# Kernel optimization log

Measured on AMD Instinct MI355X. Metric: run time of the kernel, lower is better.

## Reference

```python
import jax, jax.numpy as jnp
import numpy as np

# Model dims (rexgen/WLN canonical hyperparameters)
B, N, MAXNB, NBONDS = 16, 100, 10, 120
AF, BF, H, BIN = 82, 6, 300, 11
DEPTH, K = 3, 80


def setup_inputs() -> dict:
    key = jax.random.key(0)
    ks = jax.random.split(key, 24)
    f32 = jnp.float32
    inp = {}
    inp["fatoms"] = jax.random.normal(ks[0], (B, N, AF), f32)
    inp["fbonds"] = jax.random.normal(ks[1], (B, NBONDS, BF), f32)
    inp["atom_nb"] = jax.random.randint(ks[2], (B, N, MAXNB), 0, N)
    inp["bond_nb"] = jax.random.randint(ks[3], (B, N, MAXNB), 0, NBONDS)
    inp["num_nbs"] = jnp.full((B, N), MAXNB, jnp.int32)
    inp["n_atoms"] = jnp.full((B,), N, jnp.int32)
    inp["binary_feats"] = jax.random.normal(ks[4], (B, N, N, BIN), f32)
    inp["mask_neis"] = (jax.random.uniform(ks[5], (B, N, MAXNB, 1)) > 0.2).astype(f32)
    inp["mask_atoms"] = jnp.ones((B, N, 1), f32)
    # sparse_idx enumerates all (sample, atom_i, atom_j) pairs in row-major order
    sb = jnp.repeat(jnp.arange(B), N * N)
    si = jnp.tile(jnp.repeat(jnp.arange(N), N), B)
    sj = jnp.tile(jnp.arange(N), B * N)
    inp["sparse_idx"] = jnp.stack([sb, si, sj], axis=1).astype(jnp.int32)

    def w(k, shape):
        return jax.random.normal(k, shape, f32) * 0.1

    # WLNet params
    inp["W_atom"] = w(ks[6], (AF, H))
    inp["W_nei_atom"] = w(ks[7], (H, H))
    inp["W_nei_bond"] = w(ks[8], (BF, H))
    inp["W_self"] = w(ks[9], (H, H))
    inp["W_U2"] = w(ks[10], (H + BF, H)); inp["b_U2"] = jnp.zeros((H,), f32)
    inp["W_U1"] = w(ks[11], (2 * H, H)); inp["b_U1"] = jnp.zeros((H,), f32)
    # Attention params
    inp["W_att_local"] = w(ks[12], (H, H))
    inp["W_att_bin"] = w(ks[13], (BIN, H)); inp["b_att"] = jnp.zeros((H,), f32)
    inp["W_att_score"] = w(ks[14], (H, 1)); inp["b_att_score"] = jnp.zeros((1,), f32)
    # ReactivityScoring params
    inp["W_pl"] = w(ks[15], (H, H))
    inp["W_pg"] = w(ks[16], (H, H))
    inp["W_pb"] = w(ks[17], (BIN, H)); inp["b_p"] = jnp.zeros((H,), f32)
    inp["W_out"] = w(ks[18], (H, 1)); inp["b_out"] = jnp.zeros((1,), f32)
    return inp


def _pair_scores(fatoms, fbonds, binary_feats, mask_neis, mask_atoms,
                 W_atom, W_nei_atom, W_nei_bond, W_self, W_U2, b_U2, W_U1, b_U1,
                 W_att_local, W_att_bin, b_att, W_att_score, b_att_score,
                 W_pl, W_pg, W_pb, b_p, W_out, b_out,
                 atom_nb, bond_nb, sparse_idx):
    bidx = jnp.arange(B)[:, None, None]
    # --- WLNet graph convolution ---
    h = jax.nn.relu(fatoms @ W_atom)                       # [B,N,H]
    local = h
    for _ in range(DEPTH):
        fnei_atom = h[bidx, atom_nb]                       # [B,N,MAXNB,H]
        fnei_bond = fbonds[bidx, bond_nb]                  # [B,N,MAXNB,BF]
        h_nei = (fnei_atom @ W_nei_atom) * (fnei_bond @ W_nei_bond)
        f_nei = (h_nei * mask_neis).sum(axis=2)            # [B,N,H]
        f_self = h @ W_self
        local = f_nei * f_self * mask_atoms                # kernel output
        nei_label = jax.nn.relu(jnp.concatenate([fnei_atom, fnei_bond], -1) @ W_U2 + b_U2)
        nei_label = (nei_label * mask_neis).sum(axis=2)
        h = jax.nn.relu(jnp.concatenate([h, nei_label], -1) @ W_U1 + b_U1)
    # --- Global attention over atom pairs ---
    pair = local[:, :, None, :] + local[:, None, :, :]     # [B,N,N,H]
    att_h = jax.nn.relu(pair @ W_att_local + binary_feats @ W_att_bin + b_att)
    att_s = jax.nn.sigmoid(att_h @ W_att_score + b_att_score)  # [B,N,N,1]
    ctx = jnp.einsum('bij,bjh->bih', att_s[..., 0], local)     # [B,N,H]
    # --- Gather sparse pairs and score reactivity ---
    sb, si, sj = sparse_idx[:, 0], sparse_idx[:, 1], sparse_idx[:, 2]
    local_pair = local[sb, si] + local[sb, sj]             # [P,H]
    global_pair = ctx[sb, si] + ctx[sb, sj]                # [P,H]
    bin_pair = binary_feats[sb, si, sj]                    # [P,BIN]
    hid = jax.nn.relu(local_pair @ W_pl + global_pair @ W_pg + bin_pair @ W_pb + b_p)
    return hid @ W_out + b_out                             # [P,1]


def reference(fatoms, fbonds, atom_nb, bond_nb, num_nbs, n_atoms, binary_feats,
              mask_neis, mask_atoms, sparse_idx,
              W_atom, W_nei_atom, W_nei_bond, W_self, W_U2, b_U2, W_U1, b_U1,
              W_att_local, W_att_bin, b_att, W_att_score, b_att_score,
              W_pl, W_pg, W_pb, b_p, W_out, b_out):
    pair_scores = _pair_scores(fatoms, fbonds, binary_feats, mask_neis, mask_atoms,
                               W_atom, W_nei_atom, W_nei_bond, W_self, W_U2, b_U2, W_U1, b_U1,
                               W_att_local, W_att_bin, b_att, W_att_score, b_att_score,
                               W_pl, W_pg, W_pb, b_p, W_out, b_out,
                               atom_nb, bond_nb, sparse_idx)
    # Segmented top-k: sparse_idx rows are grouped & ordered by sample with
    # exactly N*N pairs each, so per-sample flatten == reshape to [B, N*N].
    _, topks = jax.lax.top_k(pair_scores.reshape(B, N * N), K)  # indices, matching torch.topk[1]
    return pair_scores, topks
```

## Files before the change

kernel.cpp:

```cpp
#include <hip/hip_runtime.h>
#include <hip/hip_bf16.h>
#include <math.h>

#define BB 16
#define NN 100
#define MAXNB 10
#define NBONDS 120
#define AF 82
#define BF 6
#define HH 300
#define BIN 11
#define DEPTH 3
#define KTOP 80

typedef __attribute__((ext_vector_type(8))) short short8;
typedef __attribute__((ext_vector_type(4))) float floatx4;

__device__ __forceinline__ unsigned short f2bf(float f) {
    unsigned int u = __float_as_uint(f);
    unsigned int r = (u + 0x7FFFu + ((u >> 16) & 1u)) >> 16;
    return (unsigned short)r;
}
__device__ __forceinline__ float bf2f(unsigned short h) {
    return __uint_as_float(((unsigned int)h) << 16);
}

#define O_WATOM 0
#define O_WNB   29184
#define O_U2B   38912
#define O_WNA   48640
#define O_U2A   145920
#define O_WSELF 243200
#define O_U1A   340480
#define O_U1B   437760
#define O_WATT  535040
#define O_WPL   632320
#define O_WPG   729600

__global__ __launch_bounds__(256) void k_prep(
    const float* __restrict__ s0, const float* __restrict__ s1,
    const float* __restrict__ s2, const float* __restrict__ s3,
    const float* __restrict__ s4, const float* __restrict__ s5,
    const float* __restrict__ s6, const float* __restrict__ s7,
    const float* __restrict__ s8, const float* __restrict__ s9,
    const float* __restrict__ s10,
    unsigned short* __restrict__ WTh, unsigned short* __restrict__ WTl,
    const float* __restrict__ fatoms, const float* __restrict__ fbonds,
    unsigned short* __restrict__ fatomsbf, unsigned short* __restrict__ fbondsbf,
    const float* __restrict__ bin, unsigned short* __restrict__ BINBF,
    const float* __restrict__ Wbin0, const float* __restrict__ Wbin1,
    unsigned short* __restrict__ WBF0, unsigned short* __restrict__ WBF1)
{
    const int z = blockIdx.z;
    if (z == 11) {
        int idx = blockIdx.x * 256 + threadIdx.x;
        if (idx < 1600 * 96) {
            int r = idx / 96, c = idx - r * 96;
            float f = (c < AF) ? fatoms[r * AF + c] : 0.f;
            unsigned short hb = f2bf(f);
            fatomsbf[r * 192 + c]      = hb;
            fatomsbf[r * 192 + 96 + c] = f2bf(f - bf2f(hb));
        } else {
            int i2 = idx - 1600 * 96;
            if (i2 < 1920 * 32) {
                int r = i2 / 32, c = i2 - r * 32;
                float f = (c < BF) ? fbonds[r * BF + c] : 0.f;
                unsigned short hb = f2bf(f);
                fbondsbf[r * 64 + c]      = hb;
                fbondsbf[r * 64 + 32 + c] = f2bf(f - bf2f(hb));
            }
        }
        return;
    }
    if (z == 12) {
        const int bx = blockIdx.x;
        if (bx < 625) {
            int p = bx * 256 + threadIdx.x;
            if (p < BB * NN * NN) {
                const float* src = bin + (size_t)p * BIN;
                unsigned short tmp[16];
#pragma unroll
                for (int k = 0; k < BIN; k++) tmp[k] = f2bf(src[k]);
#pragma unroll
                for (int k = BIN; k < 16; k++) tmp[k] = 0;
                *(uint4*)(BINBF + (size_t)p * 16) = *(uint4*)tmp;
                *(uint4*)(BINBF + (size_t)p * 16 + 8) = *(uint4*)(tmp + 8);
            }
        } else if (bx < 663) {
            int zb = bx - 625;
            const float* src = (zb >= 19) ? Wbin1 : Wbin0;
            unsigned short* dst = (zb >= 19) ? WBF1 : WBF0;
            int idx = (zb % 19) * 256 + threadIdx.x;
            int jj = idx & 7;
            int koct = (idx >> 3) & 1;
            int n = (idx >> 4) & 15;
            int ch = idx >> 8;
            int k = koct * 8 + jj;
            int h = ch * 16 + n;
            float f = (k < BIN && h < 300) ? src[k * 300 + h] : 0.f;
            dst[idx] = f2bf(f);
        }
        return;
    }
    const float* src; int K, kc, off;
    switch (z) {
        case 0:  src = s0;  K = AF;  kc = 3;  off = O_WATOM; break;
        case 1:  src = s1;  K = BF;  kc = 1;  off = O_WNB;   break;
        case 2:  src = s2;  K = BF;  kc = 1;  off = O_U2B;   break;
        case 3:  src = s3;  K = HH;  kc = 10; off = O_WNA;   break;
        case 4:  src = s4;  K = HH;  kc = 10; off = O_U2A;   break;
        case 5:  src = s5;  K = HH;  kc = 10; off = O_WSELF; break;
        case 6:  src = s6;  K = HH;  kc = 10; off = O_U1A;   break;
        case 7:  src = s7;  K = HH;  kc = 10; off = O_U1B;   break;
        case 8:  src = s8;  K = HH;  kc = 10; off = O_WATT;  break;
        case 9:  src = s9;  K = HH;  kc = 10; off = O_WPL;   break;
        default: src = s10; K = HH;  kc = 10; off = O_WPG;   break;
    }
    const int lim = 9728 * kc;
    int i = blockIdx.x * 256 + threadIdx.x;
    if (i < lim) {
        int jj = i & 7;
        int lane = (i >> 3) & 63;
        int rem = i >> 9;
        int kci = rem % kc;
        int ct = rem / kc;
        int k = kci * 32 + (lane >> 4) * 8 + jj;
        int col = ct * 16 + (lane & 15);
        float f = (k < K && col < 300) ? src[k * 300 + col] : 0.f;
        unsigned short hb = f2bf(f);
        WTh[off + i] = hb;
        WTl[off + i] = f2bf(f - bf2f(hb));
    }
}

__device__ __forceinline__ void gemm_core(
    const unsigned short* __restrict__ A, int lda, int kc, int M,
    const unsigned short* __restrict__ wthB, const unsigned short* __restrict__ wtlB,
    float* __restrict__ C, int ldc,
    const float* __restrict__ bias,
    const float* __restrict__ Add, int ldAdd, int addOff,
    int act, unsigned short* __restrict__ Cbf,
    int row0, int gcolBase)
{
    __shared__ unsigned short sa[16 * 648];
    if (row0 >= M) return;
    const int tid = threadIdx.x;
    const int lane = tid & 63;
    const int wid = tid >> 6;
    const int sR = kc * 64 + 8;

    {
        const uint4* Ag = (const uint4*)A;
        uint4* sa4 = (uint4*)sa;
        const int q4 = kc * 8;
        const int lda4 = lda >> 3;
        const int sR4 = q4 + 1;
        for (int i = tid; i < 16 * q4; i += 256) {
            int r = i / q4, q = i - r * q4;
            sa4[r * sR4 + q] = Ag[(size_t)(row0 + r) * lda4 + q];
        }
    }
    __syncthreads();

    const int ct = blockIdx.y * 4 + wid;
    if (ct >= 19) return;

    const int m = lane & 15;
    const int rq = lane >> 4;
    const int koct8 = rq * 8;
    const unsigned short* wth = wthB + (size_t)ct * kc * 512;
    const unsigned short* wtl = wtlB + (size_t)ct * kc * 512;

    floatx4 acc = {0.f, 0.f, 0.f, 0.f};
    for (int kci = 0; kci < kc; kci++) {
        short8 ah = *(const short8*)(sa + m * sR + kci * 32 + koct8);
        short8 al = *(const short8*)(sa + m * sR + kc * 32 + kci * 32 + koct8);
        short8 wh = *(const short8*)(wth + (kci * 64 + lane) * 8);
        short8 wl = *(const short8*)(wtl + (kci * 64 + lane) * 8);
        acc = __builtin_amdgcn_mfma_f32_16x16x32_bf16(ah, wl, acc, 0, 0, 0);
        acc = __builtin_amdgcn_mfma_f32_16x16x32_bf16(al, wh, acc, 0, 0, 0);
        acc = __builtin_amdgcn_mfma_f32_16x16x32_bf16(ah, wh, acc, 0, 0, 0);
    }

    const int col = ct * 16 + m;
    if (col < 300) {
        const float bv = bias ? bias[col] : 0.f;
        const int gcol = gcolBase + col;
#pragma unroll
        for (int r = 0; r < 4; r++) {
            const int grow = row0 + rq * 4 + r;
            float v = acc[r] + bv;
            if (Add) v += Add[(size_t)grow * ldAdd + addOff + col];
            if (act) v = fmaxf(v, 0.f);
            if (C) C[(size_t)grow * ldc + gcol] = v;
            if (Cbf) {
                unsigned short hb = f2bf(v);
                Cbf[(size_t)grow * 640 + col]       = hb;
                Cbf[(size_t)grow * 640 + 320 + col] = f2bf(v - bf2f(hb));
            }
        }
    }
}

__global__ __launch_bounds__(256) void k_gemm_mfma(
    const unsigned short* __restrict__ A, int lda, int kc, int M,
    const unsigned short* __restrict__ WTh, const unsigned short* __restrict__ WTl,
    int wtStride,
    float* __restrict__ C, int ldc,
    const float* __restrict__ bias,
    const float* __restrict__ Add, int ldAdd, int addOff,
    int act, unsigned short* __restrict__ Cbf)
{
    const int widx = blockIdx.z;
    gemm_core(A, lda, kc, M,
              WTh + (size_t)widx * wtStride, WTl + (size_t)widx * wtStride,
              C, ldc, bias, Add, ldAdd, addOff, act, Cbf,
              blockIdx.x * 16, widx * 300);
}

__global__ __launch_bounds__(256) void k_gemm_first(
    const unsigned short* __restrict__ fatomsbf,
    const unsigned short* __restrict__ fbondsbf,
    const unsigned short* __restrict__ WTh, const unsigned short* __restrict__ WTl,
    unsigned short* __restrict__ hbf, float* __restrict__ FBout)
{
    const int z = blockIdx.z;
    if (z == 0) {
        gemm_core(fatomsbf, 192, 3, 1600,
                  WTh + O_WATOM, WTl + O_WATOM,
                  nullptr, 0, nullptr, nullptr, 0, 0, 1, hbf,
                  blockIdx.x * 16, 0);
    } else {
        const int w = z - 1;
        gemm_core(fbondsbf, 64, 1, 1920,
                  WTh + O_WNB + w * 9728, WTl + O_WNB + w * 9728,
                  FBout, 600, nullptr, nullptr, 0, 0, 0, nullptr,
                  blockIdx.x * 16, w * 300);
    }
}

__global__ __launch_bounds__(320) void k_neighbor(
    const float* __restrict__ HW, const float* __restrict__ FB,
    const int* __restrict__ atom_nb, const int* __restrict__ bond_nb,
    const float* __restrict__ mask_neis, const float* __restrict__ mask_atoms,
    const float* __restrict__ b_U2,
    unsigned short* __restrict__ localbf, unsigned short* __restrict__ nlbf)
{
    __shared__ int   sAn[4][MAXNB];
    __shared__ int   sBd[4][MAXNB];
    __shared__ float sM[4][MAXNB];
    const int tx = threadIdx.x;
    const int ty = threadIdx.y;
    const int bx = blockIdx.x;
    const int bn0 = ((bx & 15) * 25 + (bx >> 4)) * 4;
    const int flat = ty * 80 + tx;

    if (flat < 40)        sAn[flat / 10][flat % 10] = atom_nb[(bn0 + flat / 10) * MAXNB + flat % 10];
    else if (flat < 80)  { int f = flat - 40; sBd[f / 10][f % 10] = bond_nb[(bn0 + f / 10) * MAXNB + f % 10]; }
    else if (flat < 120) { int f = flat - 80; sM[f / 10][f % 10]  = mask_neis[(bn0 + f / 10) * MAXNB + f % 10]; }
    __syncthreads();

    if (tx >= 75) return;
    const int bn = bn0 + ty;
    const int b = bn / NN;
    const int h4 = tx;

    const float4* HW4 = (const float4*)HW;
    const float4* FB4 = (const float4*)FB;
    const float4 bu = ((const float4*)b_U2)[h4];

    float4 fnei = make_float4(0.f,0.f,0.f,0.f);
    float4 nls  = fnei;
#pragma unroll
    for (int k = 0; k < MAXNB; k++) {
        const int an = sAn[ty][k];
        const int bd = sBd[ty][k];
        const float m = sM[ty][k];
        const float4* hr = HW4 + (size_t)(b * NN + an) * 300;
        const float4* fr = FB4 + (size_t)(b * NBONDS + bd) * 150;
        float4 ha = hr[h4];
        float4 hu = hr[75 + h4];
        float4 fa = fr[h4];
        float4 fu = fr[75 + h4];
        fnei.x = fmaf(m, ha.x * fa.x, fnei.x);
        fnei.y = fmaf(m, ha.y * fa.y, fnei.y);
        fnei.z = fmaf(m, ha.z * fa.z, fnei.z);
        fnei.w = fmaf(m, ha.w * fa.w, fnei.w);
        float ux = hu.x + fu.x + bu.x;
        float uy = hu.y + fu.y + bu.y;
        float uz = hu.z + fu.z + bu.z;
        float uw = hu.w + fu.w + bu.w;
        nls.x = fmaf(m, fmaxf(ux, 0.f), nls.x);
        nls.y = fmaf(m, fmaxf(uy, 0.f), nls.y);
        nls.z = fmaf(m, fmaxf(uz, 0.f), nls.z);
        nls.w = fmaf(m, fmaxf(uw, 0.f), nls.w);
    }
    const float ma = mask_atoms[bn];
    const float4 sf = HW4[(size_t)bn * 300 + 150 + h4];
    float lv[4], nv[4];
    lv[0] = fnei.x * sf.x * ma; lv[1] = fnei.y * sf.y * ma;
    lv[2] = fnei.z * sf.z * ma; lv[3] = fnei.w * sf.w * ma;
    nv[0] = nls.x; nv[1] = nls.y; nv[2] = nls.z; nv[3] = nls.w;

    ushort4 lh, ll, nh, nl2;
    unsigned short* lhp = (unsigned short*)&lh;
    unsigned short* llp = (unsigned short*)&ll;
    unsigned short* nhp = (unsigned short*)&nh;
    unsigned short* nlp = (unsigned short*)&nl2;
#pragma unroll
    for (int c = 0; c < 4; c++) {
        unsigned short hb = f2bf(lv[c]);
        lhp[c] = hb; llp[c] = f2bf(lv[c] - bf2f(hb));
        unsigned short nb = f2bf(nv[c]);
        nhp[c] = nb; nlp[c] = f2bf(nv[c] - bf2f(nb));
    }
    *(ushort4*)(localbf + (size_t)bn * 640 + h4 * 4)       = lh;
    *(ushort4*)(localbf + (size_t)bn * 640 + 320 + h4 * 4) = ll;
    *(ushort4*)(nlbf    + (size_t)bn * 640 + h4 * 4)       = nh;
    *(ushort4*)(nlbf    + (size_t)bn * 640 + 320 + h4 * 4) = nl2;
}

__global__ __launch_bounds__(256) void k_pair(
    const float* __restrict__ R, int ldr,
    const unsigned short* __restrict__ BINBF,
    const unsigned short* __restrict__ WBF,
    const float* __restrict__ bvec,
    const float* __restrict__ Wscore, const float* __restrict__ bscore,
    float* __restrict__ outp, int mode)
{
    __shared__ float sLi[16 * 308];
    __shared__ float sLj[16 * 308];

    const int b  = blockIdx.x;
    const int i0 = blockIdx.y * 16;
    const int j0 = blockIdx.z * 16;
    const int tid = threadIdx.x;
    const int lane = tid & 63;
    const int wid = tid >> 6;

    for (int idx = tid; idx < 16 * 308; idx += 256) {
        int r = idx / 308;
        int c = idx - r * 308;
        float vi = 0.f, vj = 0.f;
        if (c < 300) {
            if (i0 + r < NN) vi = R[(size_t)(b * NN + i0 + r) * ldr + c] + bvec[c];
            if (j0 + r < NN) vj = R[(size_t)(b * NN + j0 + r) * ldr + c];
        }
        sLi[idx] = vi;
        sLj[idx] = vj;
    }

    const int m = lane & 15;
    const int koct = lane >> 4;
    short8 afrag[4];
#pragma unroll
    for (int g = 0; g < 4; g++) {
        int ii = i0 + wid * 4 + g; if (ii > NN - 1) ii = NN - 1;
        int jj2 = j0 + m;          if (jj2 > NN - 1) jj2 = NN - 1;
        const size_t pidx = (size_t)((b * NN + ii) * NN + jj2);
        afrag[g] = *(const short8*)(BINBF + pidx * 16 + (koct & 1) * 8);
        if (koct >= 2) afrag[g] = short8{0,0,0,0,0,0,0,0};
    }
    __syncthreads();

    const int n = lane & 15;
    const int rquad = lane >> 4;
    const floatx4 zero = {0.f, 0.f, 0.f, 0.f};
    float su[4][4];
#pragma unroll
    for (int g = 0; g < 4; g++)
#pragma unroll
        for (int r = 0; r < 4; r++) su[g][r] = 0.f;

    for (int ch = 0; ch < 19; ch++) {
        const int h0 = ch * 16;
        short8 bfrag = {0,0,0,0,0,0,0,0};
        if (lane < 32)
            bfrag = *(const short8*)(WBF + ch * 256 + (n * 2 + koct) * 8);
        float wsv = 0.f;
        if (h0 + n < 300) wsv = Wscore[h0 + n];
#pragma unroll
        for (int g = 0; g < 4; g++) {
            floatx4 P = __builtin_amdgcn_mfma_f32_16x16x32_bf16(
                afrag[g], bfrag, zero, 0, 0, 0);
            const float liv = sLi[(wid * 4 + g) * 308 + h0 + n];
#pragma unroll
            for (int r = 0; r < 4; r++) {
                const float ljv = sLj[(rquad * 4 + r) * 308 + h0 + n];
                float u = P[r] + liv + ljv;
                su[g][r] = fmaf(fmaxf(u, 0.f), wsv, su[g][r]);
            }
        }
    }

    const float bs = bscore[0];
#pragma unroll
    for (int g = 0; g < 4; g++) {
#pragma unroll
        for (int r = 0; r < 4; r++) {
            float v = su[g][r];
            v += __shfl_xor(v, 1);
            v += __shfl_xor(v, 2);
            v += __shfl_xor(v, 4);
            v += __shfl_xor(v, 8);
            if (n == 0) {
                const int i = i0 + wid * 4 + g;
                const int j = j0 + rquad * 4 + r;
                if (i < NN && j < NN) {
                    float s = v + bs;
                    outp[(size_t)(b * NN + i) * NN + j] =
                        (mode == 0) ? (1.f / (1.f + expf(-s))) : s;
                }
            }
        }
    }
}

__global__ __launch_bounds__(320) void k_ctx(
    const float* __restrict__ att, const unsigned short* __restrict__ localbf,
    unsigned short* __restrict__ ctxbf)
{
    const int bx = blockIdx.x;
    const int b = bx & 15;
    const int i0 = (bx >> 4) * 4;
    const int tid = threadIdx.x;
    __shared__ float sa[4 * NN];
    for (int idx = tid; idx < 4 * NN; idx += 320) {
        int ii = idx / NN, j = idx - ii * NN;
        sa[idx] = att[(size_t)(b * NN + i0 + ii) * NN + j];
    }
    __syncthreads();
    if (tid < HH) {
        float acc0 = 0.f, acc1 = 0.f, acc2 = 0.f, acc3 = 0.f;
        for (int j = 0; j < NN; j++) {
            const unsigned short* lr = localbf + (size_t)(b * NN + j) * 640;
            float lv = bf2f(lr[tid]) + bf2f(lr[320 + tid]);
            acc0 = fmaf(sa[j], lv, acc0);
            acc1 = fmaf(sa[NN + j], lv, acc1);
            acc2 = fmaf(sa[2 * NN + j], lv, acc2);
            acc3 = fmaf(sa[3 * NN + j], lv, acc3);
        }
        float vals[4] = {acc0, acc1, acc2, acc3};
#pragma unroll
        for (int k = 0; k < 4; k++) {
            unsigned short hb = f2bf(vals[k]);
            ctxbf[(size_t)(b * NN + i0 + k) * 640 + tid]       = hb;
            ctxbf[(size_t)(b * NN + i0 + k) * 640 + 320 + tid] = f2bf(vals[k] - bf2f(hb));
        }
    }
}

__global__ __launch_bounds__(1024) void k_topk(
    const float* __restrict__ scores, float* __restrict__ topk_out)
{
    const int b = blockIdx.x;
    const int tid = threadIdx.x;
    const int wid = tid >> 6;
    const int lane = tid & 63;
    const float* sc = scores + (size_t)b * (NN * NN);

    __shared__ unsigned int skey[NN * NN];
    __shared__ unsigned int whist[16 * 256];
    __shared__ unsigned int hist[256];
    __shared__ unsigned int candU[KTOP];
    __shared__ int candI[KTOP];
    __shared__ int cntG;
    __shared__ int curMin;
    __shared__ unsigned int sh_pref, sh_mask;
    __shared__ int sh_kRem;
    __shared__ int sh_last;

    for (int idx = tid; idx < NN * NN; idx += 1024) {
        unsigned int u = __float_as_uint(sc[idx]);
        u = (u & 0x80000000u) ? ~u : (u | 0x80000000u);
        skey[idx] = u;
    }
    if (tid == 0) {
        sh_pref = 0u; sh_mask = 0u; sh_kRem = KTOP; cntG = 0; sh_last = -1;
    }
    __syncthreads();

    for (int pass = 0; pass < 4; pass++) {
        const int shift = 24 - 8 * pass;
        unsigned int* wh = whist + (wid << 8);
        wh[lane] = 0u; wh[lane + 64] = 0u; wh[lane + 128] = 0u; wh[lane + 192] = 0u;
        __syncthreads();
        const unsigned int pref = sh_pref, mask = sh_mask;
        for (int idx = tid; idx < NN * NN; idx += 1024) {
            unsigned int u = skey[idx];
            if ((u & mask) == pref)
                atomicAdd(&wh[(u >> shift) & 255u], 1u);
        }
        __syncthreads();
        if (tid < 256) {
            unsigned int s = 0u;
#pragma unroll
            for (int w = 0; w < 16; w++) s += whist[(w << 8) | tid];
            hist[tid] = s;
        }
        __syncthreads();
        if (wid == 0) {
            unsigned int h0 = hist[lane * 4 + 0];
            unsigned int h1 = hist[lane * 4 + 1];
            unsigned int h2 = hist[lane * 4 + 2];
            unsigned int h3 = hist[lane * 4 + 3];
            unsigned int own = h0 + h1 + h2 + h3;
            unsigned int suf = own;
#pragma unroll
            for (int off = 1; off < 64; off <<= 1) {
                unsigned int v = __shfl_down(suf, off);
                if (lane + off < 64) suf += v;
            }
            const int k = sh_kRem;
            const unsigned int above = suf - own;
            if (above < (unsigned int)k && suf >= (unsigned int)k) {
                unsigned int c = above, hb; int bsel;
                c += h3;
                if ((int)c >= k) { bsel = lane * 4 + 3; hb = h3; }
                else { c += h2;
                    if ((int)c >= k) { bsel = lane * 4 + 2; hb = h2; }
                    else { c += h1;
                        if ((int)c >= k) { bsel = lane * 4 + 1; hb = h1; }
                        else { c += h0; bsel = lane * 4; hb = h0; } } }
                sh_kRem = k - (int)(c - hb);
                sh_pref = pref | ((unsigned int)bsel << shift);
                sh_mask = mask | (0xFFu << shift);
            }
        }
        __syncthreads();
    }
    const unsigned int T = sh_pref;

    for (int idx = tid; idx < NN * NN; idx += 1024) {
        unsigned int u = skey[idx];
        if (u > T) {
            int pos = atomicAdd(&cntG, 1);
            candU[pos] = u;
            candI[pos] = idx;
        }
    }
    __syncthreads();
    const int needE = KTOP - cntG;

    for (int e = 0; e < needE; e++) {
        if (tid == 0) curMin = 0x7fffffff;
        __syncthreads();
        const int last = sh_last;
        for (int idx = tid; idx < NN * NN; idx += 1024) {
            if (skey[idx] == T && idx > last)
                atomicMin(&curMin, idx);
        }
        __syncthreads();
        if (tid == 0) {
            candU[cntG + e] = T;
            candI[cntG + e] = curMin;
            sh_last = curMin;
        }
        __syncthreads();
    }

    if (tid < KTOP) {
        const unsigned int mu = candU[tid];
        const int mi = candI[tid];
        int rank = 0;
        for (int o = 0; o < KTOP; o++) {
            unsigned int ou = candU[o];
            int oi = candI[o];
            if (ou > mu || (ou == mu && oi < mi)) rank++;
        }
        topk_out[b * KTOP + rank] = (float)mi;
    }
}

extern "C" void kernel_launch(void* const* d_in, const int* in_sizes, int n_in,
                              void* d_out, int out_size, void* d_ws, size_t ws_size,
                              hipStream_t stream) {
    const float* fatoms       = (const float*)d_in[0];
    const float* fbonds       = (const float*)d_in[1];
    const int*   atom_nb      = (const int*)d_in[2];
    const int*   bond_nb      = (const int*)d_in[3];
    const float* binary_feats = (const float*)d_in[6];
    const float* mask_neis    = (const float*)d_in[7];
    const float* mask_atoms   = (const float*)d_in[8];
    const float* W_atom       = (const float*)d_in[10];
    const float* W_nei_atom   = (const float*)d_in[11];
    const float* W_nei_bond   = (const float*)d_in[12];
    const float* W_self       = (const float*)d_in[13];
    const float* W_U2         = (const float*)d_in[14];
    const float* b_U2         = (const float*)d_in[15];
    const float* W_U1         = (const float*)d_in[16];
    const float* b_U1         = (const float*)d_in[17];
    const float* W_att_local  = (const float*)d_in[18];
    const float* W_att_bin    = (const float*)d_in[19];
    const float* b_att        = (const float*)d_in[20];
    const float* W_att_score  = (const float*)d_in[21];
    const float* b_att_score  = (const float*)d_in[22];
    const float* W_pl         = (const float*)d_in[23];
    const float* W_pg         = (const float*)d_in[24];
    const float* W_pb         = (const float*)d_in[25];
    const float* b_p          = (const float*)d_in[26];
    const float* W_out        = (const float*)d_in[27];
    const float* b_out        = (const float*)d_in[28];

    float* ws = (float*)d_ws;
    float* HW  = ws;
    float* FB  = HW + 1920000;
    float* LL  = FB + 1152000;
    float* LPG = LL + 960000;
    float* att = LPG + 480000;
    unsigned short* S0       = (unsigned short*)(ws + 4672000);
    unsigned short* hbf      = S0;
    unsigned short* nlbf     = S0 + 1024000;
    unsigned short* localbf  = S0 + 2048000;
    unsigned short* WTh      = S0 + 3072000;
    unsigned short* WTl      = S0 + 3898880;
    unsigned short* ctxbf    = S0 + 4725760;
    unsigned short* BINBF    = S0 + 5749760;
    unsigned short* WBF_att  = S0 + 8309760;
    unsigned short* WBF_fin  = S0 + 8314624;
    unsigned short* fatomsbf = S0 + 8319488;
    unsigned short* fbondsbf = S0 + 8626688;

    float* out = (float*)d_out;
    float* topk_out = out + (size_t)BB * NN * NN;

    k_prep<<<dim3(840, 1, 13), 256, 0, stream>>>(
        W_atom, W_nei_bond, W_U2 + 300 * 300, W_nei_atom, W_U2, W_self,
        W_U1, W_U1 + 300 * 300, W_att_local, W_pl, W_pg, WTh, WTl,
        fatoms, fbonds, fatomsbf, fbondsbf,
        binary_feats, BINBF, W_att_bin, W_pb, WBF_att, WBF_fin);

    k_gemm_first<<<dim3(120, 5, 3), 256, 0, stream>>>(
        fatomsbf, fbondsbf, WTh, WTl, hbf, FB);

    for (int d = 0; d < DEPTH; d++) {
        int nW = (d == DEPTH - 1) ? 3 : 4;
        k_gemm_mfma<<<dim3(104, 5, nW), 256, 0, stream>>>(
            hbf, 640, 10, 1600, WTh + O_WNA, WTl + O_WNA, 97280,
            HW, 1200, nullptr, nullptr, 0, 0, 0, nullptr);
        k_neighbor<<<dim3(400), dim3(80, 4), 0, stream>>>(
            HW, FB, atom_nb, bond_nb, mask_neis, mask_atoms, b_U2,
            localbf, nlbf);
        if (d < DEPTH - 1) {
            k_gemm_mfma<<<dim3(104, 5, 1), 256, 0, stream>>>(
                nlbf, 640, 10, 1600, WTh + O_U1B, WTl + O_U1B, 0,
                nullptr, 0, b_U1, HW, 1200, 900, 1, hbf);
        }
    }

    k_gemm_mfma<<<dim3(104, 5, 2), 256, 0, stream>>>(
        localbf, 640, 10, 1600, WTh + O_WATT, WTl + O_WATT, 97280,
        LL, 600, nullptr, nullptr, 0, 0, 0, nullptr);

    k_pair<<<dim3(16, 7, 7), 256, 0, stream>>>(
        LL, 600, BINBF, WBF_att, b_att, W_att_score, b_att_score,
        att, 0);

    k_ctx<<<dim3(BB * 25), 320, 0, stream>>>(att, localbf, ctxbf);

    k_gemm_mfma<<<dim3(104, 5, 1), 256, 0, stream>>>(
        ctxbf, 640, 10, 1600, WTh + O_WPG, WTl + O_WPG, 0,
        LPG, 300, nullptr, LL, 600, 300, 0, nullptr);

    k_pair<<<dim3(16, 7, 7), 256, 0, stream>>>(
        LPG, 300, BINBF, WBF_fin, b_p, W_out, b_out,
        out, 1);

    k_topk<<<dim3(BB), 1024, 0, stream>>>(out, topk_out);
}
```

Baseline: 295.4 us.

## Fuse U1 matmul into neighbor kernel and reassociate context projection

The U1 neighbor-label GEMM is folded into the neighbor aggregation kernel: each block stages its 4 rows of summed neighbor labels in shared memory and multiplies them by the FP32 W_U1 lower half with scalar FMAs. This removes a separate bf16-split MFMA launch per depth and the nlbf round trip. The context projection is reassociated as att·(local·W_pg), so W_pg joins the batched local GEMM and k_ctx writes LPG directly, dropping the ctx GEMM launch and its buffer. The last depth also skips the unused U2 neighbor path. In exchange, each of the 400 neighbor blocks re-streams the full 300x300 weight matrix through scalar FMAs, and the summation order changes.

```diff
diff --git a/kernel.cpp b/kernel.cpp
--- a/kernel.cpp
+++ b/kernel.cpp
@@ -43,7 +43,6 @@
     const float* __restrict__ s4, const float* __restrict__ s5,
     const float* __restrict__ s6, const float* __restrict__ s7,
     const float* __restrict__ s8, const float* __restrict__ s9,
-    const float* __restrict__ s10,
     unsigned short* __restrict__ WTh, unsigned short* __restrict__ WTl,
     const float* __restrict__ fatoms, const float* __restrict__ fbonds,
     unsigned short* __restrict__ fatomsbf, unsigned short* __restrict__ fbondsbf,
@@ -52,7 +51,7 @@
     unsigned short* __restrict__ WBF0, unsigned short* __restrict__ WBF1)
 {
     const int z = blockIdx.z;
-    if (z == 11) {
+    if (z == 10) {
         int idx = blockIdx.x * 256 + threadIdx.x;
         if (idx < 1600 * 96) {
             int r = idx / 96, c = idx - r * 96;
@@ -72,7 +71,7 @@
         }
         return;
     }
-    if (z == 12) {
+    if (z == 11) {
         const int bx = blockIdx.x;
         if (bx < 625) {
             int p = bx * 256 + threadIdx.x;
@@ -111,10 +110,9 @@
         case 4:  src = s4;  K = HH;  kc = 10; off = O_U2A;   break;
         case 5:  src = s5;  K = HH;  kc = 10; off = O_WSELF; break;
         case 6:  src = s6;  K = HH;  kc = 10; off = O_U1A;   break;
-        case 7:  src = s7;  K = HH;  kc = 10; off = O_U1B;   break;
-        case 8:  src = s8;  K = HH;  kc = 10; off = O_WATT;  break;
-        case 9:  src = s9;  K = HH;  kc = 10; off = O_WPL;   break;
-        default: src = s10; K = HH;  kc = 10; off = O_WPG;   break;
+        case 7:  src = s7;  K = HH;  kc = 10; off = O_WATT;  break;
+        case 8:  src = s8;  K = HH;  kc = 10; off = O_WPL;   break;
+        default: src = s9;  K = HH;  kc = 10; off = O_WPG;   break;
     }
     const int lim = 9728 * kc;
     int i = blockIdx.x * 256 + threadIdx.x;
@@ -243,12 +241,15 @@
     const float* __restrict__ HW, const float* __restrict__ FB,
     const int* __restrict__ atom_nb, const int* __restrict__ bond_nb,
     const float* __restrict__ mask_neis, const float* __restrict__ mask_atoms,
-    const float* __restrict__ b_U2,
-    unsigned short* __restrict__ localbf, unsigned short* __restrict__ nlbf)
+    const float* __restrict__ b_U2, const float* __restrict__ WU1B,
+    const float* __restrict__ b_U1,
+    unsigned short* __restrict__ localbf, unsigned short* __restrict__ hbf,
+    int computeU1)
 {
     __shared__ int   sAn[4][MAXNB];
     __shared__ int   sBd[4][MAXNB];
     __shared__ float sM[4][MAXNB];
+    __shared__ float sNL[4][300];
     const int tx = threadIdx.x;
     const int ty = threadIdx.y;
     const int bx = blockIdx.x;
@@ -260,64 +261,91 @@
     else if (flat < 120) { int f = flat - 80; sM[f / 10][f % 10]  = mask_neis[(bn0 + f / 10) * MAXNB + f % 10]; }
     __syncthreads();
 
-    if (tx >= 75) return;
-    const int bn = bn0 + ty;
-    const int b = bn / NN;
-    const int h4 = tx;
-
-    const float4* HW4 = (const float4*)HW;
-    const float4* FB4 = (const float4*)FB;
-    const float4 bu = ((const float4*)b_U2)[h4];
-
-    float4 fnei = make_float4(0.f,0.f,0.f,0.f);
-    float4 nls  = fnei;
-#pragma unroll
-    for (int k = 0; k < MAXNB; k++) {
-        const int an = sAn[ty][k];
-        const int bd = sBd[ty][k];
-        const float m = sM[ty][k];
-        const float4* hr = HW4 + (size_t)(b * NN + an) * 300;
-        const float4* fr = FB4 + (size_t)(b * NBONDS + bd) * 150;
-        float4 ha = hr[h4];
-        float4 hu = hr[75 + h4];
-        float4 fa = fr[h4];
-        float4 fu = fr[75 + h4];
-        fnei.x = fmaf(m, ha.x * fa.x, fnei.x);
-        fnei.y = fmaf(m, ha.y * fa.y, fnei.y);
-        fnei.z = fmaf(m, ha.z * fa.z, fnei.z);
-        fnei.w = fmaf(m, ha.w * fa.w, fnei.w);
-        float ux = hu.x + fu.x + bu.x;
-        float uy = hu.y + fu.y + bu.y;
-        float uz = hu.z + fu.z + bu.z;
-        float uw = hu.w + fu.w + bu.w;
-        nls.x = fmaf(m, fmaxf(ux, 0.f), nls.x);
-        nls.y = fmaf(m, fmaxf(uy, 0.f), nls.y);
-        nls.z = fmaf(m, fmaxf(uz, 0.f), nls.z);
-        nls.w = fmaf(m, fmaxf(uw, 0.f), nls.w);
-    }
-    const float ma = mask_atoms[bn];
-    const float4 sf = HW4[(size_t)bn * 300 + 150 + h4];
-    float lv[4], nv[4];
-    lv[0] = fnei.x * sf.x * ma; lv[1] = fnei.y * sf.y * ma;
-    lv[2] = fnei.z * sf.z * ma; lv[3] = fnei.w * sf.w * ma;
-    nv[0] = nls.x; nv[1] = nls.y; nv[2] = nls.z; nv[3] = nls.w;
-
-    ushort4 lh, ll, nh, nl2;
-    unsigned short* lhp = (unsigned short*)&lh;
-    unsigned short* llp = (unsigned short*)&ll;
-    unsigned short* nhp = (unsigned short*)&nh;
-    unsigned short* nlp = (unsigned short*)&nl2;
-#pragma unroll
-    for (int c = 0; c < 4; c++) {
-        unsigned short hb = f2bf(lv[c]);
-        lhp[c] = hb; llp[c] = f2bf(lv[c] - bf2f(hb));
-        unsigned short nb = f2bf(nv[c]);
-        nhp[c] = nb; nlp[c] = f2bf(nv[c] - bf2f(nb));
-    }
-    *(ushort4*)(localbf + (size_t)bn * 640 + h4 * 4)       = lh;
-    *(ushort4*)(localbf + (size_t)bn * 640 + 320 + h4 * 4) = ll;
-    *(ushort4*)(nlbf    + (size_t)bn * 640 + h4 * 4)       = nh;
-    *(ushort4*)(nlbf    + (size_t)bn * 640 + 320 + h4 * 4) = nl2;
+    if (tx < 75) {
+        const int bn = bn0 + ty;
+        const int b = bn / NN;
+        const int h4 = tx;
+
+        const float4* HW4 = (const float4*)HW;
+        const float4* FB4 = (const float4*)FB;
+        const float4 bu = ((const float4*)b_U2)[h4];
+
+        float4 fnei = make_float4(0.f,0.f,0.f,0.f);
+        float4 nls  = fnei;
+#pragma unroll
+        for (int k = 0; k < MAXNB; k++) {
+            const int an = sAn[ty][k];
+            const int bd = sBd[ty][k];
+            const float m = sM[ty][k];
+            const float4* hr = HW4 + (size_t)(b * NN + an) * 300;
+            const float4* fr = FB4 + (size_t)(b * NBONDS + bd) * 150;
+            float4 ha = hr[h4];
+            float4 fa = fr[h4];
+            fnei.x = fmaf(m, ha.x * fa.x, fnei.x);
+            fnei.y = fmaf(m, ha.y * fa.y, fnei.y);
+            fnei.z = fmaf(m, ha.z * fa.z, fnei.z);
+            fnei.w = fmaf(m, ha.w * fa.w, fnei.w);
+            if (computeU1) {
+                float4 hu = hr[75 + h4];
+                float4 fu = fr[75 + h4];
+                float ux = hu.x + fu.x + bu.x;
+                float uy = hu.y + fu.y + bu.y;
+                float uz = hu.z + fu.z + bu.z;
+                float uw = hu.w + fu.w + bu.w;
+                nls.x = fmaf(m, fmaxf(ux, 0.f), nls.x);
+                nls.y = fmaf(m, fmaxf(uy, 0.f), nls.y);
+                nls.z = fmaf(m, fmaxf(uz, 0.f), nls.z);
+                nls.w = fmaf(m, fmaxf(uw, 0.f), nls.w);
+            }
+        }
+        const float ma = mask_atoms[bn];
+        const float4 sf = HW4[(size_t)bn * 300 + 150 + h4];
+        float lv[4];
+        lv[0] = fnei.x * sf.x * ma; lv[1] = fnei.y * sf.y * ma;
+        lv[2] = fnei.z * sf.z * ma; lv[3] = fnei.w * sf.w * ma;
+
+        ushort4 lh, ll;
+        unsigned short* lhp = (unsigned short*)&lh;
+        unsigned short* llp = (unsigned short*)&ll;
+#pragma unroll
+        for (int c = 0; c < 4; c++) {
+            unsigned short hb = f2bf(lv[c]);
+            lhp[c] = hb; llp[c] = f2bf(lv[c] - bf2f(hb));
+        }
+        *(ushort4*)(localbf + (size_t)bn * 640 + h4 * 4)       = lh;
+        *(ushort4*)(localbf + (size_t)bn * 640 + 320 + h4 * 4) = ll;
+
+        if (computeU1) {
+            sNL[ty][h4 * 4 + 0] = nls.x;
+            sNL[ty][h4 * 4 + 1] = nls.y;
+            sNL[ty][h4 * 4 + 2] = nls.z;
+            sNL[ty][h4 * 4 + 3] = nls.w;
+        }
+    }
+    if (!computeU1) return;
+    __syncthreads();
+
+    if (flat < 300) {
+        float a0 = 0.f, a1 = 0.f, a2 = 0.f, a3 = 0.f;
+#pragma unroll 4
+        for (int k = 0; k < 300; k++) {
+            const float w = WU1B[k * 300 + flat];
+            a0 = fmaf(sNL[0][k], w, a0);
+            a1 = fmaf(sNL[1][k], w, a1);
+            a2 = fmaf(sNL[2][k], w, a2);
+            a3 = fmaf(sNL[3][k], w, a3);
+        }
+        const float bb = b_U1[flat];
+        float av[4] = {a0, a1, a2, a3};
+#pragma unroll
+        for (int r = 0; r < 4; r++) {
+            float v = HW[(size_t)(bn0 + r) * 1200 + 900 + flat] + bb + av[r];
+            v = fmaxf(v, 0.f);
+            unsigned short hb = f2bf(v);
+            hbf[(size_t)(bn0 + r) * 640 + flat]       = hb;
+            hbf[(size_t)(bn0 + r) * 640 + 320 + flat] = f2bf(v - bf2f(hb));
+        }
+    }
 }
 
 __global__ __launch_bounds__(256) void k_pair(
@@ -417,8 +445,8 @@
 }
 
 __global__ __launch_bounds__(320) void k_ctx(
-    const float* __restrict__ att, const unsigned short* __restrict__ localbf,
-    unsigned short* __restrict__ ctxbf)
+    const float* __restrict__ att, const float* __restrict__ LL,
+    float* __restrict__ LPG)
 {
     const int bx = blockIdx.x;
     const int b = bx & 15;
@@ -433,8 +461,7 @@
     if (tid < HH) {
         float acc0 = 0.f, acc1 = 0.f, acc2 = 0.f, acc3 = 0.f;
         for (int j = 0; j < NN; j++) {
-            const unsigned short* lr = localbf + (size_t)(b * NN + j) * 640;
-            float lv = bf2f(lr[tid]) + bf2f(lr[320 + tid]);
+            const float lv = LL[(size_t)(b * NN + j) * 900 + 600 + tid];
             acc0 = fmaf(sa[j], lv, acc0);
             acc1 = fmaf(sa[NN + j], lv, acc1);
             acc2 = fmaf(sa[2 * NN + j], lv, acc2);
@@ -443,9 +470,8 @@
         float vals[4] = {acc0, acc1, acc2, acc3};
 #pragma unroll
         for (int k = 0; k < 4; k++) {
-            unsigned short hb = f2bf(vals[k]);
-            ctxbf[(size_t)(b * NN + i0 + k) * 640 + tid]       = hb;
-            ctxbf[(size_t)(b * NN + i0 + k) * 640 + 320 + tid] = f2bf(vals[k] - bf2f(hb));
+            LPG[(size_t)(b * NN + i0 + k) * 300 + tid] =
+                vals[k] + LL[(size_t)(b * NN + i0 + k) * 900 + 300 + tid];
         }
     }
 }
@@ -606,27 +632,25 @@
     float* HW  = ws;
     float* FB  = HW + 1920000;
     float* LL  = FB + 1152000;
-    float* LPG = LL + 960000;
+    float* LPG = LL + 1440000;
     float* att = LPG + 480000;
-    unsigned short* S0       = (unsigned short*)(ws + 4672000);
+    unsigned short* S0       = (unsigned short*)(ws + 5152000);
     unsigned short* hbf      = S0;
-    unsigned short* nlbf     = S0 + 1024000;
-    unsigned short* localbf  = S0 + 2048000;
-    unsigned short* WTh      = S0 + 3072000;
-    unsigned short* WTl      = S0 + 3898880;
-    unsigned short* ctxbf    = S0 + 4725760;
-    unsigned short* BINBF    = S0 + 5749760;
-    unsigned short* WBF_att  = S0 + 8309760;
-    unsigned short* WBF_fin  = S0 + 8314624;
-    unsigned short* fatomsbf = S0 + 8319488;
-    unsigned short* fbondsbf = S0 + 8626688;
+    unsigned short* localbf  = S0 + 1024000;
+    unsigned short* WTh      = S0 + 2048000;
+    unsigned short* WTl      = S0 + 2874880;
+    unsigned short* BINBF    = S0 + 3701760;
+    unsigned short* WBF_att  = S0 + 6261760;
+    unsigned short* WBF_fin  = S0 + 6266624;
+    unsigned short* fatomsbf = S0 + 6271488;
+    unsigned short* fbondsbf = S0 + 6578688;
 
     float* out = (float*)d_out;
     float* topk_out = out + (size_t)BB * NN * NN;
 
-    k_prep<<<dim3(840, 1, 13), 256, 0, stream>>>(
+    k_prep<<<dim3(840, 1, 12), 256, 0, stream>>>(
         W_atom, W_nei_bond, W_U2 + 300 * 300, W_nei_atom, W_U2, W_self,
-        W_U1, W_U1 + 300 * 300, W_att_local, W_pl, W_pg, WTh, WTl,
+        W_U1, W_att_local, W_pl, W_pg, WTh, WTl,
         fatoms, fbonds, fatomsbf, fbondsbf,
         binary_feats, BINBF, W_att_bin, W_pb, WBF_att, WBF_fin);
 
@@ -640,27 +664,19 @@
             HW, 1200, nullptr, nullptr, 0, 0, 0, nullptr);
         k_neighbor<<<dim3(400), dim3(80, 4), 0, stream>>>(
             HW, FB, atom_nb, bond_nb, mask_neis, mask_atoms, b_U2,
-            localbf, nlbf);
-        if (d < DEPTH - 1) {
-            k_gemm_mfma<<<dim3(104, 5, 1), 256, 0, stream>>>(
-                nlbf, 640, 10, 1600, WTh + O_U1B, WTl + O_U1B, 0,
-                nullptr, 0, b_U1, HW, 1200, 900, 1, hbf);
-        }
-    }
-
-    k_gemm_mfma<<<dim3(104, 5, 2), 256, 0, stream>>>(
+            W_U1 + 300 * 300, b_U1, localbf, hbf,
+            (d < DEPTH - 1) ? 1 : 0);
+    }
+
+    k_gemm_mfma<<<dim3(104, 5, 3), 256, 0, stream>>>(
         localbf, 640, 10, 1600, WTh + O_WATT, WTl + O_WATT, 97280,
-        LL, 600, nullptr, nullptr, 0, 0, 0, nullptr);
+        LL, 900, nullptr, nullptr, 0, 0, 0, nullptr);
 
     k_pair<<<dim3(16, 7, 7), 256, 0, stream>>>(
-        LL, 600, BINBF, WBF_att, b_att, W_att_score, b_att_score,
+        LL, 900, BINBF, WBF_att, b_att, W_att_score, b_att_score,
         att, 0);
 
-    k_ctx<<<dim3(BB * 25), 320, 0, stream>>>(att, localbf, ctxbf);
-
-    k_gemm_mfma<<<dim3(104, 5, 1), 256, 0, stream>>>(
-        ctxbf, 640, 10, 1600, WTh + O_WPG, WTl + O_WPG, 0,
-        LPG, 300, nullptr, LL, 600, 300, 0, nullptr);
+    k_ctx<<<dim3(BB * 25), 320, 0, stream>>>(att, LL, LPG);
 
     k_pair<<<dim3(16, 7, 7), 256, 0, stream>>>(
         LPG, 300, BINBF, WBF_fin, b_p, W_out, b_out,
```

After: 314.4 us. 6.4% more time.

## Reassociate context projection into the attention GEMM and skip unused final neighbor work

Applied to the files above, without the earlier changes.

Uses (att·local)·W_pg = att·(local·W_pg). The local·W_pg product is computed as a third output slab of the existing attention GEMM, so k_ctx now multiplies attention weights directly with that fp32 result and adds the local projection. This removes the separate ctx GEMM launch and the split-bf16 ctx buffer. k_neighbor also skips the U1 message computation and nlbf writes on the last depth iteration, where they are never used, and two kernels get min-blocks launch bounds. The change relies on the W_pg weights sitting right after the attention weights in the transposed weight buffer. It also changes rounding, since ctx is no longer rounded before the projection.

```diff
diff --git a/kernel.cpp b/kernel.cpp
--- a/kernel.cpp
+++ b/kernel.cpp
@@ -239,12 +239,13 @@
     }
 }
 
-__global__ __launch_bounds__(320) void k_neighbor(
+__global__ __launch_bounds__(320, 2) void k_neighbor(
     const float* __restrict__ HW, const float* __restrict__ FB,
     const int* __restrict__ atom_nb, const int* __restrict__ bond_nb,
     const float* __restrict__ mask_neis, const float* __restrict__ mask_atoms,
     const float* __restrict__ b_U2,
-    unsigned short* __restrict__ localbf, unsigned short* __restrict__ nlbf)
+    unsigned short* __restrict__ localbf, unsigned short* __restrict__ nlbf,
+    int computeU1)
 {
     __shared__ int   sAn[4][MAXNB];
     __shared__ int   sBd[4][MAXNB];
@@ -267,57 +268,79 @@
 
     const float4* HW4 = (const float4*)HW;
     const float4* FB4 = (const float4*)FB;
-    const float4 bu = ((const float4*)b_U2)[h4];
 
     float4 fnei = make_float4(0.f,0.f,0.f,0.f);
     float4 nls  = fnei;
-#pragma unroll
-    for (int k = 0; k < MAXNB; k++) {
-        const int an = sAn[ty][k];
-        const int bd = sBd[ty][k];
-        const float m = sM[ty][k];
-        const float4* hr = HW4 + (size_t)(b * NN + an) * 300;
-        const float4* fr = FB4 + (size_t)(b * NBONDS + bd) * 150;
-        float4 ha = hr[h4];
-        float4 hu = hr[75 + h4];
-        float4 fa = fr[h4];
-        float4 fu = fr[75 + h4];
-        fnei.x = fmaf(m, ha.x * fa.x, fnei.x);
-        fnei.y = fmaf(m, ha.y * fa.y, fnei.y);
-        fnei.z = fmaf(m, ha.z * fa.z, fnei.z);
-        fnei.w = fmaf(m, ha.w * fa.w, fnei.w);
-        float ux = hu.x + fu.x + bu.x;
-        float uy = hu.y + fu.y + bu.y;
-        float uz = hu.z + fu.z + bu.z;
-        float uw = hu.w + fu.w + bu.w;
-        nls.x = fmaf(m, fmaxf(ux, 0.f), nls.x);
-        nls.y = fmaf(m, fmaxf(uy, 0.f), nls.y);
-        nls.z = fmaf(m, fmaxf(uz, 0.f), nls.z);
-        nls.w = fmaf(m, fmaxf(uw, 0.f), nls.w);
+    if (computeU1) {
+        const float4 bu = ((const float4*)b_U2)[h4];
+#pragma unroll
+        for (int k = 0; k < MAXNB; k++) {
+            const int an = sAn[ty][k];
+            const int bd = sBd[ty][k];
+            const float m = sM[ty][k];
+            const float4* hr = HW4 + (size_t)(b * NN + an) * 300;
+            const float4* fr = FB4 + (size_t)(b * NBONDS + bd) * 150;
+            float4 ha = hr[h4];
+            float4 hu = hr[75 + h4];
+            float4 fa = fr[h4];
+            float4 fu = fr[75 + h4];
+            fnei.x = fmaf(m, ha.x * fa.x, fnei.x);
+            fnei.y = fmaf(m, ha.y * fa.y, fnei.y);
+            fnei.z = fmaf(m, ha.z * fa.z, fnei.z);
+            fnei.w = fmaf(m, ha.w * fa.w, fnei.w);
+            float ux = hu.x + fu.x + bu.x;
+            float uy = hu.y + fu.y + bu.y;
+            float uz = hu.z + fu.z + bu.z;
+            float uw = hu.w + fu.w + bu.w;
+            nls.x = fmaf(m, fmaxf(ux, 0.f), nls.x);
+            nls.y = fmaf(m, fmaxf(uy, 0.f), nls.y);
+            nls.z = fmaf(m, fmaxf(uz, 0.f), nls.z);
+            nls.w = fmaf(m, fmaxf(uw, 0.f), nls.w);
+        }
+    } else {
+#pragma unroll
+        for (int k = 0; k < MAXNB; k++) {
+            const int an = sAn[ty][k];
+            const int bd = sBd[ty][k];
+            const float m = sM[ty][k];
+            float4 ha = HW4[(size_t)(b * NN + an) * 300 + h4];
+            float4 fa = FB4[(size_t)(b * NBONDS + bd) * 150 + h4];
+            fnei.x = fmaf(m, ha.x * fa.x, fnei.x);
+            fnei.y = fmaf(m, ha.y * fa.y, fnei.y);
+            fnei.z = fmaf(m, ha.z * fa.z, fnei.z);
+            fnei.w = fmaf(m, ha.w * fa.w, fnei.w);
+        }
     }
     const float ma = mask_atoms[bn];
     const float4 sf = HW4[(size_t)bn * 300 + 150 + h4];
-    float lv[4], nv[4];
+    float lv[4];
     lv[0] = fnei.x * sf.x * ma; lv[1] = fnei.y * sf.y * ma;
     lv[2] = fnei.z * sf.z * ma; lv[3] = fnei.w * sf.w * ma;
-    nv[0] = nls.x; nv[1] = nls.y; nv[2] = nls.z; nv[3] = nls.w;
-
-    ushort4 lh, ll, nh, nl2;
+
+    ushort4 lh, ll;
     unsigned short* lhp = (unsigned short*)&lh;
     unsigned short* llp = (unsigned short*)&ll;
-    unsigned short* nhp = (unsigned short*)&nh;
-    unsigned short* nlp = (unsigned short*)&nl2;
 #pragma unroll
     for (int c = 0; c < 4; c++) {
         unsigned short hb = f2bf(lv[c]);
         lhp[c] = hb; llp[c] = f2bf(lv[c] - bf2f(hb));
-        unsigned short nb = f2bf(nv[c]);
-        nhp[c] = nb; nlp[c] = f2bf(nv[c] - bf2f(nb));
     }
     *(ushort4*)(localbf + (size_t)bn * 640 + h4 * 4)       = lh;
     *(ushort4*)(localbf + (size_t)bn * 640 + 320 + h4 * 4) = ll;
-    *(ushort4*)(nlbf    + (size_t)bn * 640 + h4 * 4)       = nh;
-    *(ushort4*)(nlbf    + (size_t)bn * 640 + 320 + h4 * 4) = nl2;
+
+    if (computeU1) {
+        float nv[4] = {nls.x, nls.y, nls.z, nls.w};
+        ushort4 nh, nl2;
+        unsigned short* nhp = (unsigned short*)&nh;
+        unsigned short* nlp = (unsigned short*)&nl2;
+#pragma unroll
+        for (int c = 0; c < 4; c++) {
+            unsigned short nb = f2bf(nv[c]);
+            nhp[c] = nb; nlp[c] = f2bf(nv[c] - bf2f(nb));
+        }
+        *(ushort4*)(nlbf + (size_t)bn * 640 + h4 * 4)       = nh;
+        *(ushort4*)(nlbf + (size_t)bn * 640 + 320 + h4 * 4) = nl2;
+    }
 }
 
 __global__ __launch_bounds__(256) void k_pair(
@@ -416,9 +439,9 @@
     }
 }
 
-__global__ __launch_bounds__(320) void k_ctx(
-    const float* __restrict__ att, const unsigned short* __restrict__ localbf,
-    unsigned short* __restrict__ ctxbf)
+__global__ __launch_bounds__(320, 2) void k_ctx(
+    const float* __restrict__ att, const float* __restrict__ LL,
+    float* __restrict__ LPG)
 {
     const int bx = blockIdx.x;
     const int b = bx & 15;
@@ -432,9 +455,9 @@
     __syncthreads();
     if (tid < HH) {
         float acc0 = 0.f, acc1 = 0.f, acc2 = 0.f, acc3 = 0.f;
+#pragma unroll 4
         for (int j = 0; j < NN; j++) {
-            const unsigned short* lr = localbf + (size_t)(b * NN + j) * 640;
-            float lv = bf2f(lr[tid]) + bf2f(lr[320 + tid]);
+            const float lv = LL[(size_t)(b * NN + j) * 900 + 600 + tid];
             acc0 = fmaf(sa[j], lv, acc0);
             acc1 = fmaf(sa[NN + j], lv, acc1);
             acc2 = fmaf(sa[2 * NN + j], lv, acc2);
@@ -443,9 +466,8 @@
         float vals[4] = {acc0, acc1, acc2, acc3};
 #pragma unroll
         for (int k = 0; k < 4; k++) {
-            unsigned short hb = f2bf(vals[k]);
-            ctxbf[(size_t)(b * NN + i0 + k) * 640 + tid]       = hb;
-            ctxbf[(size_t)(b * NN + i0 + k) * 640 + 320 + tid] = f2bf(vals[k] - bf2f(hb));
+            LPG[(size_t)(b * NN + i0 + k) * 300 + tid] =
+                vals[k] + LL[(size_t)(b * NN + i0 + k) * 900 + 300 + tid];
         }
     }
 }
@@ -606,20 +628,19 @@
     float* HW  = ws;
     float* FB  = HW + 1920000;
     float* LL  = FB + 1152000;
-    float* LPG = LL + 960000;
+    float* LPG = LL + 1440000;
     float* att = LPG + 480000;
-    unsigned short* S0       = (unsigned short*)(ws + 4672000);
+    unsigned short* S0       = (unsigned short*)(ws + 5152000);
     unsigned short* hbf      = S0;
     unsigned short* nlbf     = S0 + 1024000;
     unsigned short* localbf  = S0 + 2048000;
     unsigned short* WTh      = S0 + 3072000;
     unsigned short* WTl      = S0 + 3898880;
-    unsigned short* ctxbf    = S0 + 4725760;
-    unsigned short* BINBF    = S0 + 5749760;
-    unsigned short* WBF_att  = S0 + 8309760;
-    unsigned short* WBF_fin  = S0 + 8314624;
-    unsigned short* fatomsbf = S0 + 8319488;
-    unsigned short* fbondsbf = S0 + 8626688;
+    unsigned short* BINBF    = S0 + 4725760;
+    unsigned short* WBF_att  = S0 + 7285760;
+    unsigned short* WBF_fin  = S0 + 7290624;
+    unsigned short* fatomsbf = S0 + 7295488;
+    unsigned short* fbondsbf = S0 + 7602688;
 
     float* out = (float*)d_out;
     float* topk_out = out + (size_t)BB * NN * NN;
@@ -640,7 +661,7 @@
             HW, 1200, nullptr, nullptr, 0, 0, 0, nullptr);
         k_neighbor<<<dim3(400), dim3(80, 4), 0, stream>>>(
             HW, FB, atom_nb, bond_nb, mask_neis, mask_atoms, b_U2,
-            localbf, nlbf);
+            localbf, nlbf, (d < DEPTH - 1) ? 1 : 0);
         if (d < DEPTH - 1) {
             k_gemm_mfma<<<dim3(104, 5, 1), 256, 0, stream>>>(
                 nlbf, 640, 10, 1600, WTh + O_U1B, WTl + O_U1B, 0,
@@ -648,19 +669,15 @@
         }
     }
 
-    k_gemm_mfma<<<dim3(104, 5, 2), 256, 0, stream>>>(
+    k_gemm_mfma<<<dim3(104, 5, 3), 256, 0, stream>>>(
         localbf, 640, 10, 1600, WTh + O_WATT, WTl + O_WATT, 97280,
-        LL, 600, nullptr, nullptr, 0, 0, 0, nullptr);
+        LL, 900, nullptr, nullptr, 0, 0, 0, nullptr);
 
     k_pair<<<dim3(16, 7, 7), 256, 0, stream>>>(
-        LL, 600, BINBF, WBF_att, b_att, W_att_score, b_att_score,
+        LL, 900, BINBF, WBF_att, b_att, W_att_score, b_att_score,
         att, 0);
 
-    k_ctx<<<dim3(BB * 25), 320, 0, stream>>>(att, localbf, ctxbf);
-
-    k_gemm_mfma<<<dim3(104, 5, 1), 256, 0, stream>>>(
-        ctxbf, 640, 10, 1600, WTh + O_WPG, WTl + O_WPG, 0,
-        LPG, 300, nullptr, LL, 600, 300, 0, nullptr);
+    k_ctx<<<dim3(BB * 25), 320, 0, stream>>>(att, LL, LPG);
 
     k_pair<<<dim3(16, 7, 7), 256, 0, stream>>>(
         LPG, 300, BINBF, WBF_fin, b_p, W_out, b_out,
```

After: 292.8 us. Within noise of the previous version (-0.9%).
